# Performance work log

Measured on AMD Instinct MI355X. Metric: run time of the kernel, lower is better.

Reference implementation:

```python
import jax, jax.numpy as jnp
import numpy as np

B, L, D, H, DH = 2, 2048, 768, 12, 3072
HD = D // H          # head dim = 64
EPS = 1e-6
SCALE = float(np.sqrt(HD))


def setup_inputs() -> dict:
    key = jax.random.key(0)
    ks = jax.random.split(key, 24)
    w = lambda k, shape: jax.random.normal(k, shape, jnp.float32) * 0.02
    # RoPE angles: [L, HD//2]
    inv_freq = 1.0 / (10000.0 ** (jnp.arange(HD // 2, dtype=jnp.float32) / (HD // 2)))
    ang = jnp.arange(L, dtype=jnp.float32)[:, None] * inv_freq[None, :]
    return {
        "x": jax.random.normal(ks[0], (B, L, D), jnp.float32),
        "c": jax.random.normal(ks[1], (B, D), jnp.float32),
        "freqs_cos": jnp.cos(ang),
        "freqs_sin": jnp.sin(ang),
        "W_q": w(ks[2], (D, D)), "W_k": w(ks[3], (D, D)),
        "W_v": w(ks[4], (D, D)), "W_o": w(ks[5], (D, D)),
        "cond_w1": w(ks[6], (D, DH)), "cond_b1": jnp.zeros((DH,), jnp.float32),
        "cond_w2": w(ks[7], (DH, D)), "cond_b2": jnp.zeros((D,), jnp.float32),
        "attn_norm_w": jnp.ones((D,), jnp.float32),
        "attn_alpha": w(ks[8], (D, D)), "attn_beta": w(ks[9], (D, D)),
        "attn_gamma": w(ks[10], (D, D)),
        "ffn_gate": w(ks[11], (D, DH)), "ffn_hidden": w(ks[12], (D, DH)),
        "ffn_out": w(ks[13], (DH, D)),
        "ffn_norm_w": jnp.ones((D,), jnp.float32),
        "ffn_beta": w(ks[14], (D, D)), "ffn_gamma": w(ks[15], (D, D)),
    }


def _rms_norm(x, w):
    return w * x * jax.lax.rsqrt(jnp.mean(x * x, axis=-1, keepdims=True) + EPS)


def _rope(x, cos, sin):
    # x: [b, n, l, hd]; complex pairs are consecutive (even, odd) lanes
    x0, x1 = x[..., 0::2], x[..., 1::2]
    c, s = cos[None, None], sin[None, None]          # [1,1,l,hd//2]
    r0 = x0 * c - x1 * s
    r1 = x0 * s + x1 * c
    return jnp.stack([r0, r1], axis=-1).reshape(x.shape)


def _attention(h, cos, sin, W_q, W_k, W_v, W_o):
    b, l, d = h.shape
    split = lambda y: y.reshape(b, l, H, HD).transpose(0, 2, 1, 3)  # b n l hd
    q = _rope(split(h @ W_q), cos, sin)
    k = _rope(split(h @ W_k), cos, sin)
    v = split(h @ W_v)
    scores = jnp.einsum("bnld,bnmd->bnlm", q, k) / SCALE
    attn = jax.nn.softmax(scores, axis=-1)
    o = jnp.einsum("bnlm,bnmd->bnld", attn, v)
    return o.transpose(0, 2, 1, 3).reshape(b, l, d) @ W_o


def reference(x, c, freqs_cos, freqs_sin, W_q, W_k, W_v, W_o,
              cond_w1, cond_b1, cond_w2, cond_b2,
              attn_norm_w, attn_alpha, attn_beta, attn_gamma,
              ffn_gate, ffn_hidden, ffn_out, ffn_norm_w, ffn_beta, ffn_gamma):
    # conditioning embedding
    c2 = jax.nn.silu(c @ cond_w1 + cond_b1) @ cond_w2 + cond_b2   # [b, d]
    mod = lambda W: (c2 @ W)[:, None]                              # [b, 1, d]
    # attention sub-block with AdaLN modulation + alpha gating
    h = _rms_norm(x, attn_norm_w) * mod(attn_gamma) + mod(attn_beta)
    x = x + _attention(h, freqs_cos, freqs_sin, W_q, W_k, W_v, W_o) * mod(attn_alpha)
    # SwiGLU FFN sub-block (original gates the residual by ffn_gamma, not alpha)
    h = _rms_norm(x, ffn_norm_w) * mod(ffn_gamma) + mod(ffn_beta)
    ff = (jax.nn.silu(h @ ffn_gate) * (h @ ffn_hidden)) @ ffn_out
    return x + ff * mod(ffn_gamma)
```

## Files before the change

### kernel.cpp

```cpp
#include <hip/hip_runtime.h>

typedef unsigned short u16;
typedef __attribute__((ext_vector_type(8))) short short8;
typedef __attribute__((ext_vector_type(4))) float f32x4;

#define L_SEQ 2048
#define NHEAD 12
#define KVB 128
#define QBLK 128

__device__ __forceinline__ u16 f2bf(float f) {
    union { float f; unsigned u; } x; x.f = f;
    unsigned r = x.u + 0x7fffu + ((x.u >> 16) & 1u);
    return (u16)(r >> 16);
}
__device__ __forceinline__ float bf2f(u16 u) {
    union { unsigned u; float f; } x; x.u = ((unsigned)u) << 16;
    return x.f;
}
__device__ __forceinline__ float silu_f(float x) { return x / (1.f + __expf(-x)); }

__device__ __forceinline__ void gload16(const u16* g, u16* l) {
    __builtin_amdgcn_global_load_lds(
        (const __attribute__((address_space(1))) void*)g,
        (__attribute__((address_space(3))) void*)l, 16, 0, 0);
}

__global__ __launch_bounds__(256) void transpose_all(
    const float* __restrict__ S0, const float* __restrict__ S1,
    const float* __restrict__ S2, const float* __restrict__ S3,
    const float* __restrict__ S4, const float* __restrict__ S5,
    const float* __restrict__ S6,
    u16* __restrict__ D0, u16* __restrict__ D1, u16* __restrict__ D2,
    u16* __restrict__ D3, u16* __restrict__ D4, u16* __restrict__ D5,
    u16* __restrict__ D6)
{
    int id = blockIdx.x;
    const float* W; u16* Wt; int K, N, local;
    if (id < 2304) {
        int sec = id / 576; local = id - sec * 576; K = 768; N = 768;
        W  = (sec == 0) ? S0 : (sec == 1) ? S1 : (sec == 2) ? S2 : S3;
        Wt = (sec == 0) ? D0 : (sec == 1) ? D1 : (sec == 2) ? D2 : D3;
    } else if (id < 6912) {
        int sec = (id - 2304) / 2304; local = (id - 2304) - sec * 2304; K = 768; N = 3072;
        W = sec ? S5 : S4; Wt = sec ? D5 : D4;
    } else {
        local = id - 6912; K = 3072; N = 768; W = S6; Wt = D6;
    }
    int nx = N >> 5;
    int n0 = (local % nx) * 32, k0 = (local / nx) * 32;
    __shared__ float t[32][33];
    int tx = threadIdx.x & 31, ty = threadIdx.x >> 5;
#pragma unroll
    for (int i = 0; i < 4; i++)
        t[ty + 8 * i][tx] = W[(size_t)(k0 + ty + 8 * i) * N + n0 + tx];
    __syncthreads();
#pragma unroll
    for (int i = 0; i < 4; i++)
        Wt[(size_t)(n0 + ty + 8 * i) * K + k0 + tx] = f2bf(t[tx][ty + 8 * i]);
}

__global__ __launch_bounds__(256) void cond_mlp1(
    const float* __restrict__ c, const float* __restrict__ w1, float* __restrict__ part)
{
    int j = blockIdx.x * 256 + threadIdx.x;
    int d0 = blockIdx.y * 96;
    float a0 = 0.f, a1 = 0.f;
    for (int d = d0; d < d0 + 96; ++d) {
        float w = w1[(size_t)d * 3072 + j];
        a0 += c[d] * w;
        a1 += c[768 + d] * w;
    }
    part[(size_t)(blockIdx.y * 2 + 0) * 3072 + j] = a0;
    part[(size_t)(blockIdx.y * 2 + 1) * 3072 + j] = a1;
}

__global__ __launch_bounds__(256) void cond_mlp2(
    const float* __restrict__ part, const float* __restrict__ b1,
    const float* __restrict__ w2, float* __restrict__ c2part)
{
    __shared__ float hid[2][384];
    const int tid = threadIdx.x;
    const int d0 = blockIdx.y * 384;
    for (int i = tid; i < 768; i += 256) {
        int b = i / 384, dd = i - b * 384;
        float s = b1[d0 + dd];
#pragma unroll
        for (int p = 0; p < 8; p++) s += part[(size_t)(p * 2 + b) * 3072 + d0 + dd];
        hid[b][dd] = silu_f(s);
    }
    __syncthreads();
    int jj = tid & 63, kc = tid >> 6;
    int j = blockIdx.x * 64 + jj;
    float a0 = 0.f, a1 = 0.f;
    for (int dd = kc * 96; dd < kc * 96 + 96; ++dd) {
        float w = w2[(size_t)(d0 + dd) * 768 + j];
        a0 += hid[0][dd] * w;
        a1 += hid[1][dd] * w;
    }
    __shared__ float r0[256], r1[256];
    r0[tid] = a0; r1[tid] = a1;
    __syncthreads();
    if (kc == 0) {
        a0 = r0[jj] + r0[64 + jj] + r0[128 + jj] + r0[192 + jj];
        a1 = r1[jj] + r1[64 + jj] + r1[128 + jj] + r1[192 + jj];
        c2part[(size_t)(blockIdx.y * 2 + 0) * 768 + j] = a0;
        c2part[(size_t)(blockIdx.y * 2 + 1) * 768 + j] = a1;
    }
}

__global__ __launch_bounds__(256) void mod_gemm(
    const float* __restrict__ c2part, const float* __restrict__ b2,
    const float* __restrict__ W0, const float* __restrict__ W1,
    const float* __restrict__ W2, const float* __restrict__ W3,
    const float* __restrict__ W4, float* __restrict__ out)
{
    __shared__ float c2s[2][768];
    const int tid = threadIdx.x;
    for (int i = tid; i < 1536; i += 256) {
        int b = i / 768, d = i - b * 768;
        float s = b2[d];
#pragma unroll
        for (int p = 0; p < 8; p++) s += c2part[(size_t)(p * 2 + b) * 768 + d];
        c2s[b][d] = s;
    }
    __syncthreads();
    int w = blockIdx.y;
    const float* W = (w == 0) ? W0 : (w == 1) ? W1 : (w == 2) ? W2 : (w == 3) ? W3 : W4;
    int jj = tid & 63, kc = tid >> 6;
    int j = blockIdx.x * 64 + jj;
    float a0 = 0.f, a1 = 0.f;
    for (int d = kc * 192; d < kc * 192 + 192; ++d) {
        float ww = W[(size_t)d * 768 + j];
        a0 += c2s[0][d] * ww;
        a1 += c2s[1][d] * ww;
    }
    __shared__ float r0[256], r1[256];
    r0[tid] = a0; r1[tid] = a1;
    __syncthreads();
    if (kc == 0) {
        a0 = r0[jj] + r0[64 + jj] + r0[128 + jj] + r0[192 + jj];
        a1 = r1[jj] + r1[64 + jj] + r1[128 + jj] + r1[192 + jj];
        out[(size_t)(w * 2 + 0) * 768 + j] = a0;
        out[(size_t)(w * 2 + 1) * 768 + j] = a1;
    }
}

__global__ __launch_bounds__(256) void rmsnorm_mod(
    const float* __restrict__ xin, const float* __restrict__ nw,
    const float* __restrict__ gamma, const float* __restrict__ beta,
    u16* __restrict__ hout)
{
    int row = blockIdx.x;
    int b = row >> 11;
    const float* xr = xin + (size_t)row * 768;
    int t = threadIdx.x;
    float v0 = xr[t], v1 = xr[t + 256], v2 = xr[t + 512];
    float ss = v0 * v0 + v1 * v1 + v2 * v2;
#pragma unroll
    for (int m = 1; m < 64; m <<= 1) ss += __shfl_xor(ss, m);
    __shared__ float red[4];
    if ((t & 63) == 0) red[t >> 6] = ss;
    __syncthreads();
    float tot = red[0] + red[1] + red[2] + red[3];
    float rr = rsqrtf(tot * (1.f / 768.f) + 1e-6f);
    u16* ho = hout + (size_t)row * 768;
    const float* g = gamma + (size_t)b * 768;
    const float* be = beta + (size_t)b * 768;
#pragma unroll
    for (int i = 0; i < 3; i++) {
        int col = t + i * 256;
        float v = (i == 0) ? v0 : (i == 1) ? v1 : v2;
        ho[col] = f2bf(v * rr * nw[col] * g[col] + be[col]);
    }
}

template<int BM, int WM, int MODE, int LBX>
__global__ __launch_bounds__(256) void gemm_bf16(
    const u16* __restrict__ A, const u16* __restrict__ Bt,
    float* __restrict__ Cf, u16* __restrict__ Cb,
    const float* __restrict__ X, const float* __restrict__ coef,
    int M, int N, int K)
{
    constexpr int MR = WM / 16, NR = 4;
    __shared__ __align__(16) u16 As[2][BM * 32];
    __shared__ __align__(16) u16 Bs[2][128 * 32];
    const int lid = blockIdx.x;
    const int xcd = lid & 7, li = lid >> 3;
    const int bxi = xcd * (1 << LBX) + (li & ((1 << LBX) - 1));
    const int byi = li >> LBX;
    const int tid = threadIdx.x;
    const int lane = tid & 63, wid = tid >> 6;
    const int lo = lane & 15, hi = lane >> 4;
    const int bm = bxi * BM, bn = byi * 128;
    const int wrow = (wid >> 1) * WM, wcol = (wid & 1) * 64;

    f32x4 acc[MR][NR];
#pragma unroll
    for (int a = 0; a < MR; a++)
#pragma unroll
        for (int b = 0; b < NR; b++)
            acc[a][b] = (f32x4){0.f, 0.f, 0.f, 0.f};

    auto stage = [&](int buf, int k0) {
#pragma unroll
        for (int p = 0; p < BM / 64; p++) {
            int ch = tid + p * 256;
            gload16(A + (size_t)(bm + (ch >> 2)) * K + k0 + (ch & 3) * 8, &As[buf][ch * 8]);
        }
#pragma unroll
        for (int p = 0; p < 2; p++) {
            int ch = tid + p * 256;
            gload16(Bt + (size_t)(bn + (ch >> 2)) * K + k0 + (ch & 3) * 8, &Bs[buf][ch * 8]);
        }
    };

    stage(0, 0);
    int cur = 0;
    const int NT = K >> 5;
    for (int t = 0; t < NT; t++) {
        __syncthreads();
        if (t + 1 < NT) stage(cur ^ 1, (t + 1) * 32);
        short8 af[MR], bfr[NR];
#pragma unroll
        for (int mi = 0; mi < MR; mi++)
            af[mi] = *(const short8*)(&As[cur][(wrow + mi * 16 + lo) * 32 + hi * 8]);
#pragma unroll
        for (int nj = 0; nj < NR; nj++)
            bfr[nj] = *(const short8*)(&Bs[cur][(wcol + nj * 16 + lo) * 32 + hi * 8]);
        __builtin_amdgcn_s_setprio(1);
#pragma unroll
        for (int mi = 0; mi < MR; mi++)
#pragma unroll
            for (int nj = 0; nj < NR; nj++)
                acc[mi][nj] = __builtin_amdgcn_mfma_f32_16x16x32_bf16(af[mi], bfr[nj], acc[mi][nj], 0, 0, 0);
        __builtin_amdgcn_s_setprio(0);
        cur ^= 1;
    }
#pragma unroll
    for (int mi = 0; mi < MR; mi++)
#pragma unroll
        for (int nj = 0; nj < NR; nj++)
#pragma unroll
            for (int i = 0; i < 4; i++) {
                int row = bm + wrow + mi * 16 + hi * 4 + i;
                int col = bn + wcol + nj * 16 + lo;
                size_t idx = (size_t)row * N + col;
                float v = acc[mi][nj][i];
                if (MODE == 1) {
                    Cb[idx] = f2bf(v);
                } else {
                    int b = row >> 11;
                    Cf[idx] = X[idx] + v * coef[(size_t)b * N + col];
                }
            }
}

__global__ __launch_bounds__(256) void gemm_ffn1(
    const u16* __restrict__ A, const u16* __restrict__ Gt, const u16* __restrict__ Ht,
    u16* __restrict__ ff, int M, int N, int K)
{
    __shared__ __align__(16) u16 As[2][128 * 32];
    __shared__ __align__(16) u16 Gs[2][64 * 32];
    __shared__ __align__(16) u16 Hs[2][64 * 32];
    const int lid = blockIdx.x;
    const int xcd = lid & 7, li = lid >> 3;
    const int bxi = xcd * 4 + (li & 3);
    const int byi = li >> 2;
    const int tid = threadIdx.x;
    const int lane = tid & 63, wid = tid >> 6;
    const int lo = lane & 15, hi = lane >> 4;
    const int bm = bxi * 128, bn = byi * 64;
    const int wrow = (wid >> 1) * 64, wcol = (wid & 1) * 32;

    f32x4 ag[4][2], ah[4][2];
#pragma unroll
    for (int a = 0; a < 4; a++)
#pragma unroll
        for (int b = 0; b < 2; b++) {
            ag[a][b] = (f32x4){0.f, 0.f, 0.f, 0.f};
            ah[a][b] = (f32x4){0.f, 0.f, 0.f, 0.f};
        }

    auto stage = [&](int buf, int k0) {
#pragma unroll
        for (int p = 0; p < 2; p++) {
            int ch = tid + p * 256;
            gload16(A + (size_t)(bm + (ch >> 2)) * K + k0 + (ch & 3) * 8, &As[buf][ch * 8]);
        }
        {
            int ch = tid;
            gload16(Gt + (size_t)(bn + (ch >> 2)) * K + k0 + (ch & 3) * 8, &Gs[buf][ch * 8]);
            gload16(Ht + (size_t)(bn + (ch >> 2)) * K + k0 + (ch & 3) * 8, &Hs[buf][ch * 8]);
        }
    };

    stage(0, 0);
    int cur = 0;
    const int NT = K >> 5;
    for (int t = 0; t < NT; t++) {
        __syncthreads();
        if (t + 1 < NT) stage(cur ^ 1, (t + 1) * 32);
        short8 af[4], gf[2], hf[2];
#pragma unroll
        for (int mi = 0; mi < 4; mi++)
            af[mi] = *(const short8*)(&As[cur][(wrow + mi * 16 + lo) * 32 + hi * 8]);
#pragma unroll
        for (int nj = 0; nj < 2; nj++) {
            gf[nj] = *(const short8*)(&Gs[cur][(wcol + nj * 16 + lo) * 32 + hi * 8]);
            hf[nj] = *(const short8*)(&Hs[cur][(wcol + nj * 16 + lo) * 32 + hi * 8]);
        }
        __builtin_amdgcn_s_setprio(1);
#pragma unroll
        for (int mi = 0; mi < 4; mi++)
#pragma unroll
            for (int nj = 0; nj < 2; nj++) {
                ag[mi][nj] = __builtin_amdgcn_mfma_f32_16x16x32_bf16(af[mi], gf[nj], ag[mi][nj], 0, 0, 0);
                ah[mi][nj] = __builtin_amdgcn_mfma_f32_16x16x32_bf16(af[mi], hf[nj], ah[mi][nj], 0, 0, 0);
            }
        __builtin_amdgcn_s_setprio(0);
        cur ^= 1;
    }
#pragma unroll
    for (int mi = 0; mi < 4; mi++)
#pragma unroll
        for (int nj = 0; nj < 2; nj++)
#pragma unroll
            for (int i = 0; i < 4; i++) {
                int row = bm + wrow + mi * 16 + hi * 4 + i;
                int col = bn + wcol + nj * 16 + lo;
                ff[(size_t)row * N + col] = f2bf(silu_f(ag[mi][nj][i]) * ah[mi][nj][i]);
            }
}

__global__ __launch_bounds__(256) void rope_reshape(
    const u16* __restrict__ qr, const u16* __restrict__ kr, const u16* __restrict__ vr,
    const float* __restrict__ fc, const float* __restrict__ fs,
    u16* __restrict__ qo, u16* __restrict__ ko, u16* __restrict__ vt)
{
    const float QSCALE = 0.125f * 1.44269504f;
    __shared__ u16 Vl[64 * 64];
    const int tid = threadIdx.x;
    const int bh = blockIdx.y, lt = blockIdx.x;
    const int b = bh / NHEAD, h = bh % NHEAD;
    const int l0 = lt * 64;
    const int lrow = tid >> 2, ch = tid & 3;

    const size_t srow = ((size_t)(b * L_SEQ + l0 + lrow)) * 2304 + h * 64 + ch * 16;
    const size_t drow = ((size_t)(bh * L_SEQ + l0 + lrow)) * 64 + ch * 16;

    float cs[8], sn[8];
#pragma unroll
    for (int i = 0; i < 8; i++) {
        cs[i] = fc[(l0 + lrow) * 32 + ch * 8 + i];
        sn[i] = fs[(l0 + lrow) * 32 + ch * 8 + i];
    }
    union { int4 v4[2]; u16 s[16]; } iv, ov;
    iv.v4[0] = *(const int4*)(qr + srow); iv.v4[1] = *(const int4*)(qr + srow + 8);
#pragma unroll
    for (int i = 0; i < 8; i++) {
        float x0 = bf2f(iv.s[2 * i]), x1 = bf2f(iv.s[2 * i + 1]);
        ov.s[2 * i]     = f2bf((x0 * cs[i] - x1 * sn[i]) * QSCALE);
        ov.s[2 * i + 1] = f2bf((x0 * sn[i] + x1 * cs[i]) * QSCALE);
    }
    *(int4*)(qo + drow) = ov.v4[0]; *(int4*)(qo + drow + 8) = ov.v4[1];
    iv.v4[0] = *(const int4*)(kr + srow); iv.v4[1] = *(const int4*)(kr + srow + 8);
#pragma unroll
    for (int i = 0; i < 8; i++) {
        float x0 = bf2f(iv.s[2 * i]), x1 = bf2f(iv.s[2 * i + 1]);
        ov.s[2 * i]     = f2bf(x0 * cs[i] - x1 * sn[i]);
        ov.s[2 * i + 1] = f2bf(x0 * sn[i] + x1 * cs[i]);
    }
    *(int4*)(ko + drow) = ov.v4[0]; *(int4*)(ko + drow + 8) = ov.v4[1];
    iv.v4[0] = *(const int4*)(vr + srow); iv.v4[1] = *(const int4*)(vr + srow + 8);
#pragma unroll
    for (int e = 0; e < 16; e++) {
        int d = ch * 16 + e;
        Vl[d * 64 + (lrow ^ (((d >> 3) & 7) << 3))] = iv.s[e];
    }
    __syncthreads();
    const int d = tid >> 2;
    const int key = ((d >> 3) & 7) << 3;
    int4 o0 = *(const int4*)(&Vl[d * 64 + ((ch * 16) ^ key)]);
    int4 o1 = *(const int4*)(&Vl[d * 64 + ((ch * 16 + 8) ^ key)]);
    u16* vd = vt + ((size_t)bh * 64 + d) * L_SEQ + l0 + ch * 16;
    *(int4*)(vd) = o0; *(int4*)(vd + 8) = o1;
}

__global__ __launch_bounds__(512) void attn_fwd(
    const u16* __restrict__ q, const u16* __restrict__ k, const u16* __restrict__ vt,
    u16* __restrict__ outp)
{
    __shared__ __align__(16) u16 Kb[KVB * 64];
    __shared__ __align__(16) u16 Vb[64 * KVB];
    __shared__ __align__(16) u16 Ps[8][16 * KVB];
    const int tid = threadIdx.x;
    const int lane = tid & 63, wid = tid >> 6;
    const int lo = lane & 15, hi = lane >> 4;
    const int lid = blockIdx.x;
    const int xcd = lid & 7, li = lid >> 3;
    const int bh = xcd * 3 + (li >> 4);
    const int qt = li & 15;
    const int b = bh / NHEAD, h = bh % NHEAD;
    const int q0 = qt * QBLK + wid * 16;
    const u16* qb = q + ((size_t)bh * L_SEQ + q0) * 64;
    const u16* kbase = k + (size_t)bh * L_SEQ * 64;
    const u16* vbase = vt + (size_t)bh * 64 * L_SEQ;

    short8 qa0 = *(const short8*)(qb + lo * 64 + hi * 8);
    short8 qa1 = *(const short8*)(qb + lo * 64 + 32 + hi * 8);

    f32x4 oacc[4];
#pragma unroll
    for (int dt = 0; dt < 4; dt++) oacc[dt] = (f32x4){0.f, 0.f, 0.f, 0.f};
    float m_ = -1e30f, ls = 0.f;

    const int rk = tid >> 3, gk = tid & 7;
    const u16* ka = kbase + (size_t)rk * 64 + ((gk ^ (rk & 7)) * 8);
    const int rv = tid >> 4, gv = tid & 15;
    const u16* va = vbase + (size_t)rv * L_SEQ + ((gv ^ (rv & 15)) * 8);
    u16* kdst = &Kb[tid * 8];
    u16* vdst = &Vb[tid * 8];

    int4 kr0, kr1, vr0, vr1;
    kr0 = *(const int4*)(ka);
    kr1 = *(const int4*)(ka + 4096);
    vr0 = *(const int4*)(va);
    vr1 = *(const int4*)(va + 65536);

    const int NT = L_SEQ / KVB;
    u16* pw = &Ps[wid][0];
    const int pkey = lo << 3;
    for (int t = 0; t < NT; t++) {
        __syncthreads();
        *(int4*)(kdst)        = kr0;
        *(int4*)(kdst + 4096) = kr1;
        *(int4*)(vdst)        = vr0;
        *(int4*)(vdst + 4096) = vr1;
        __syncthreads();
        if (t + 1 < NT) {
            int kv0 = (t + 1) * KVB;
            const u16* kan = ka + (size_t)kv0 * 64;
            const u16* van = va + kv0;
            kr0 = *(const int4*)(kan);
            kr1 = *(const int4*)(kan + 4096);
            vr0 = *(const int4*)(van);
            vr1 = *(const int4*)(van + 65536);
        }
        f32x4 s[8];
#pragma unroll
        for (int nt = 0; nt < 8; nt++) {
            int kr_ = nt * 16 + lo;
            const u16* kp = &Kb[kr_ * 64];
            int key = (kr_ & 7) << 3;
            short8 kf0 = *(const short8*)(kp + ((hi * 8) ^ key));
            short8 kf1 = *(const short8*)(kp + ((32 + hi * 8) ^ key));
            __builtin_amdgcn_s_setprio(1);
            f32x4 z = (f32x4){0.f, 0.f, 0.f, 0.f};
            z = __builtin_amdgcn_mfma_f32_16x16x32_bf16(kf0, qa0, z, 0, 0, 0);
            s[nt] = __builtin_amdgcn_mfma_f32_16x16x32_bf16(kf1, qa1, s[nt] = z, 0, 0, 0);
            __builtin_amdgcn_s_setprio(0);
        }
        float t0 = fmaxf(fmaxf(s[0][0], s[0][1]), fmaxf(s[0][2], s[0][3]));
        float t1 = fmaxf(fmaxf(s[1][0], s[1][1]), fmaxf(s[1][2], s[1][3]));
        float t2 = fmaxf(fmaxf(s[2][0], s[2][1]), fmaxf(s[2][2], s[2][3]));
        float t3 = fmaxf(fmaxf(s[3][0], s[3][1]), fmaxf(s[3][2], s[3][3]));
        float t4 = fmaxf(fmaxf(s[4][0], s[4][1]), fmaxf(s[4][2], s[4][3]));
        float t5 = fmaxf(fmaxf(s[5][0], s[5][1]), fmaxf(s[5][2], s[5][3]));
        float t6 = fmaxf(fmaxf(s[6][0], s[6][1]), fmaxf(s[6][2], s[6][3]));
        float t7 = fmaxf(fmaxf(s[7][0], s[7][1]), fmaxf(s[7][2], s[7][3]));
        float pmax = fmaxf(fmaxf(fmaxf(t0, t1), fmaxf(t2, t3)),
                           fmaxf(fmaxf(t4, t5), fmaxf(t6, t7)));
        pmax = fmaxf(pmax, __shfl_xor(pmax, 16));
        pmax = fmaxf(pmax, __shfl_xor(pmax, 32));
        if (!__all(pmax - m_ <= 8.f)) {
            float mn = fmaxf(m_, pmax);
            float al = exp2f(m_ - mn);
            m_ = mn;
            ls *= al;
#pragma unroll
            for (int dt = 0; dt < 4; dt++) oacc[dt] *= al;
        }
        float rsA = 0.f, rsB = 0.f, rsC = 0.f, rsD = 0.f;
#pragma unroll
        for (int nt = 0; nt < 8; nt++) {
            float p0 = exp2f(s[nt][0] - m_);
            float p1 = exp2f(s[nt][1] - m_);
            float p2 = exp2f(s[nt][2] - m_);
            float p3 = exp2f(s[nt][3] - m_);
            s[nt][0] = p0; s[nt][1] = p1; s[nt][2] = p2; s[nt][3] = p3;
            rsA += p0; rsB += p1; rsC += p2; rsD += p3;
        }
        ls += (rsA + rsB) + (rsC + rsD);
#pragma unroll
        for (int nt = 0; nt < 8; nt++) {
            unsigned w0, w1;
            asm("v_cvt_pk_bf16_f32 %0, %1, %2" : "=v"(w0) : "v"(s[nt][0]), "v"(s[nt][1]));
            asm("v_cvt_pk_bf16_f32 %0, %1, %2" : "=v"(w1) : "v"(s[nt][2]), "v"(s[nt][3]));
            uint2 pk2; pk2.x = w0; pk2.y = w1;
            *(uint2*)(pw + lo * KVB + ((nt * 16 + hi * 4) ^ pkey)) = pk2;
        }
        short8 pa0 = *(const short8*)(pw + lo * KVB + ((0 * 32 + hi * 8) ^ pkey));
        short8 pa1 = *(const short8*)(pw + lo * KVB + ((1 * 32 + hi * 8) ^ pkey));
        short8 pa2 = *(const short8*)(pw + lo * KVB + ((2 * 32 + hi * 8) ^ pkey));
        short8 pa3 = *(const short8*)(pw + lo * KVB + ((3 * 32 + hi * 8) ^ pkey));
#pragma unroll
        for (int dt = 0; dt < 4; dt++) {
            int vr_ = dt * 16 + lo;
            const u16* vp = &Vb[vr_ * KVB];
            int vkey = (vr_ & 15) << 3;
            short8 vf0 = *(const short8*)(vp + ((0 * 32 + hi * 8) ^ vkey));
            short8 vf1 = *(const short8*)(vp + ((1 * 32 + hi * 8) ^ vkey));
            short8 vf2 = *(const short8*)(vp + ((2 * 32 + hi * 8) ^ vkey));
            short8 vf3 = *(const short8*)(vp + ((3 * 32 + hi * 8) ^ vkey));
            __builtin_amdgcn_s_setprio(1);
            oacc[dt] = __builtin_amdgcn_mfma_f32_16x16x32_bf16(vf0, pa0, oacc[dt], 0, 0, 0);
            oacc[dt] = __builtin_amdgcn_mfma_f32_16x16x32_bf16(vf1, pa1, oacc[dt], 0, 0, 0);
            oacc[dt] = __builtin_amdgcn_mfma_f32_16x16x32_bf16(vf2, pa2, oacc[dt], 0, 0, 0);
            oacc[dt] = __builtin_amdgcn_mfma_f32_16x16x32_bf16(vf3, pa3, oacc[dt], 0, 0, 0);
            __builtin_amdgcn_s_setprio(0);
        }
    }
    ls += __shfl_xor(ls, 16);
    ls += __shfl_xor(ls, 32);
    float inv = 1.f / ls;
    int qrow = q0 + lo;
    u16* orow = outp + ((size_t)(b * L_SEQ + qrow)) * 768 + h * 64;
#pragma unroll
    for (int dt = 0; dt < 4; dt++) {
        unsigned w0, w1;
        float o0 = oacc[dt][0] * inv, o1 = oacc[dt][1] * inv;
        float o2 = oacc[dt][2] * inv, o3 = oacc[dt][3] * inv;
        asm("v_cvt_pk_bf16_f32 %0, %1, %2" : "=v"(w0) : "v"(o0), "v"(o1));
        asm("v_cvt_pk_bf16_f32 %0, %1, %2" : "=v"(w1) : "v"(o2), "v"(o3));
        uint2 pk2; pk2.x = w0; pk2.y = w1;
        *(uint2*)(orow + dt * 16 + hi * 4) = pk2;
    }
}

extern "C" void kernel_launch(void* const* d_in, const int* in_sizes, int n_in,
                              void* d_out, int out_size, void* d_ws, size_t ws_size,
                              hipStream_t stream)
{
    const float* x      = (const float*)d_in[0];
    const float* c      = (const float*)d_in[1];
    const float* fcos   = (const float*)d_in[2];
    const float* fsin   = (const float*)d_in[3];
    const float* Wq     = (const float*)d_in[4];
    const float* Wk     = (const float*)d_in[5];
    const float* Wv     = (const float*)d_in[6];
    const float* Wo     = (const float*)d_in[7];
    const float* cw1    = (const float*)d_in[8];
    const float* cb1    = (const float*)d_in[9];
    const float* cw2    = (const float*)d_in[10];
    const float* cb2    = (const float*)d_in[11];
    const float* anw    = (const float*)d_in[12];
    const float* Walpha = (const float*)d_in[13];
    const float* Wbeta  = (const float*)d_in[14];
    const float* Wgamma = (const float*)d_in[15];
    const float* Wgate  = (const float*)d_in[16];
    const float* Whid   = (const float*)d_in[17];
    const float* Wout   = (const float*)d_in[18];
    const float* fnw    = (const float*)d_in[19];
    const float* Wbetaf = (const float*)d_in[20];
    const float* Wgammaf= (const float*)d_in[21];

    const int M = 4096;
    char* ws = (char*)d_ws;
    size_t off = 0;
    auto alloc = [&](size_t bytes) -> char* {
        char* p = ws + off;
        off += (bytes + 255) & ~(size_t)255;
        return p;
    };
    u16* wq_t   = (u16*)alloc((size_t)768 * 768 * 2);
    u16* wk_t   = (u16*)alloc((size_t)768 * 768 * 2);
    u16* wv_t   = (u16*)alloc((size_t)768 * 768 * 2);
    u16* wo_t   = (u16*)alloc((size_t)768 * 768 * 2);
    u16* gate_t = (u16*)alloc((size_t)3072 * 768 * 2);
    u16* hid_t  = (u16*)alloc((size_t)3072 * 768 * 2);
    u16* out_t  = (u16*)alloc((size_t)768 * 3072 * 2);
    float* part1 = (float*)alloc((size_t)8 * 2 * 3072 * 4);
    float* part2 = (float*)alloc((size_t)8 * 2 * 768 * 4);
    float* mods = (float*)alloc(5 * 2 * 768 * 4);
    u16* hbuf   = (u16*)alloc((size_t)M * 768 * 2);
    u16* qkvraw = (u16*)alloc((size_t)M * 2304 * 2);
    u16* qrope  = (u16*)alloc((size_t)M * 768 * 2);
    u16* krope  = (u16*)alloc((size_t)M * 768 * 2);
    u16* vtb    = (u16*)alloc((size_t)M * 768 * 2);
    u16* attnh  = (u16*)alloc((size_t)M * 768 * 2);
    float* ybuf = (float*)alloc((size_t)M * 768 * 4);
    u16* ffbuf  = (u16*)alloc((size_t)M * 3072 * 2);

    transpose_all<<<9216, 256, 0, stream>>>(
        Wq, Wk, Wv, Wo, Wgate, Whid, Wout,
        wq_t, wk_t, wv_t, wo_t, gate_t, hid_t, out_t);

    cond_mlp1<<<dim3(12, 8), 256, 0, stream>>>(c, cw1, part1);
    cond_mlp2<<<dim3(12, 8), 256, 0, stream>>>(part1, cb1, cw2, part2);
    mod_gemm<<<dim3(12, 5), 256, 0, stream>>>(
        part2, cb2, Wgamma, Wbeta, Walpha, Wgammaf, Wbetaf, mods);

    rmsnorm_mod<<<M, 256, 0, stream>>>(x, anw, mods + 0 * 1536, mods + 1 * 1536, hbuf);

    gemm_bf16<128, 64, 1, 2><<<dim3(576), 256, 0, stream>>>(
        hbuf, wq_t, nullptr, qkvraw, nullptr, nullptr, M, 2304, 768);

    rope_reshape<<<dim3(32, 24), 256, 0, stream>>>(
        qkvraw, qkvraw + 768, qkvraw + 1536,
        fcos, fsin, qrope, krope, vtb);

    attn_fwd<<<dim3(384), 512, 0, stream>>>(qrope, krope, vtb, attnh);

    gemm_bf16<64, 32, 2, 3><<<dim3(384), 256, 0, stream>>>(
        attnh, wo_t, ybuf, nullptr, x, mods + 2 * 1536, M, 768, 768);

    rmsnorm_mod<<<M, 256, 0, stream>>>(ybuf, fnw, mods + 3 * 1536, mods + 4 * 1536, hbuf);

    gemm_ffn1<<<dim3(1536), 256, 0, stream>>>(
        hbuf, gate_t, hid_t, ffbuf, M, 3072, 768);

    gemm_bf16<64, 32, 2, 3><<<dim3(384), 256, 0, stream>>>(
        ffbuf, out_t, (float*)d_out, nullptr, ybuf, mods + 3 * 1536, M, 768, 3072);
}
```

Before: 261.0 us.

## Triple-buffer LDS staging in GEMM kernels with explicit vmcnt waits

Both the generic bf16 GEMM and the fused FFN gate/hidden GEMM move from double to triple-buffered LDS tiles. Loads are now issued two K-steps ahead. The full __syncthreads is replaced by raw s_barrier plus hand-counted s_waitcnt vmcnt values, so only the oldest stage's async global-to-LDS loads must finish before compute. This is meant to hide more global-memory latency behind MFMA work. The cost is 50% more shared memory per block, which may lower occupancy, and hardcoded wait counts that depend on the per-stage load count.

```diff
diff --git a/kernel.cpp b/kernel.cpp
--- a/kernel.cpp
+++ b/kernel.cpp
@@ -183,8 +183,9 @@
     int M, int N, int K)
 {
     constexpr int MR = WM / 16, NR = 4;
-    __shared__ __align__(16) u16 As[2][BM * 32];
-    __shared__ __align__(16) u16 Bs[2][128 * 32];
+    constexpr int LPT = BM / 64 + 2;
+    __shared__ __align__(16) u16 As[3][BM * 32];
+    __shared__ __align__(16) u16 Bs[3][128 * 32];
     const int lid = blockIdx.x;
     const int xcd = lid & 7, li = lid >> 3;
     const int bxi = xcd * (1 << LBX) + (li & ((1 << LBX) - 1));
@@ -215,12 +216,24 @@
         }
     };
 
+    const int NT = K >> 5;
     stage(0, 0);
+    stage(1, 32);
     int cur = 0;
-    const int NT = K >> 5;
     for (int t = 0; t < NT; t++) {
-        __syncthreads();
-        if (t + 1 < NT) stage(cur ^ 1, (t + 1) * 32);
+        __builtin_amdgcn_s_barrier();
+        int nxt = cur + 2; if (nxt >= 3) nxt -= 3;
+        if (t + 2 < NT) stage(nxt, (t + 2) * 32);
+        if (t + 2 < NT) {
+            if constexpr (LPT == 4) asm volatile("s_waitcnt vmcnt(8)" ::: "memory");
+            else                    asm volatile("s_waitcnt vmcnt(6)" ::: "memory");
+        } else if (t + 1 < NT) {
+            if constexpr (LPT == 4) asm volatile("s_waitcnt vmcnt(4)" ::: "memory");
+            else                    asm volatile("s_waitcnt vmcnt(3)" ::: "memory");
+        } else {
+            asm volatile("s_waitcnt vmcnt(0)" ::: "memory");
+        }
+        __builtin_amdgcn_s_barrier();
         short8 af[MR], bfr[NR];
 #pragma unroll
         for (int mi = 0; mi < MR; mi++)
@@ -235,7 +248,7 @@
             for (int nj = 0; nj < NR; nj++)
                 acc[mi][nj] = __builtin_amdgcn_mfma_f32_16x16x32_bf16(af[mi], bfr[nj], acc[mi][nj], 0, 0, 0);
         __builtin_amdgcn_s_setprio(0);
-        cur ^= 1;
+        cur = (cur == 2) ? 0 : cur + 1;
     }
 #pragma unroll
     for (int mi = 0; mi < MR; mi++)
@@ -260,9 +273,9 @@
     const u16* __restrict__ A, const u16* __restrict__ Gt, const u16* __restrict__ Ht,
     u16* __restrict__ ff, int M, int N, int K)
 {
-    __shared__ __align__(16) u16 As[2][128 * 32];
-    __shared__ __align__(16) u16 Gs[2][64 * 32];
-    __shared__ __align__(16) u16 Hs[2][64 * 32];
+    __shared__ __align__(16) u16 As[3][128 * 32];
+    __shared__ __align__(16) u16 Gs[3][64 * 32];
+    __shared__ __align__(16) u16 Hs[3][64 * 32];
     const int lid = blockIdx.x;
     const int xcd = lid & 7, li = lid >> 3;
     const int bxi = xcd * 4 + (li & 3);
@@ -295,12 +308,18 @@
         }
     };
 
+    const int NT = K >> 5;
     stage(0, 0);
+    stage(1, 32);
     int cur = 0;
-    const int NT = K >> 5;
     for (int t = 0; t < NT; t++) {
-        __syncthreads();
-        if (t + 1 < NT) stage(cur ^ 1, (t + 1) * 32);
+        __builtin_amdgcn_s_barrier();
+        int nxt = cur + 2; if (nxt >= 3) nxt -= 3;
+        if (t + 2 < NT) stage(nxt, (t + 2) * 32);
+        if (t + 2 < NT)      asm volatile("s_waitcnt vmcnt(8)" ::: "memory");
+        else if (t + 1 < NT) asm volatile("s_waitcnt vmcnt(4)" ::: "memory");
+        else                 asm volatile("s_waitcnt vmcnt(0)" ::: "memory");
+        __builtin_amdgcn_s_barrier();
         short8 af[4], gf[2], hf[2];
 #pragma unroll
         for (int mi = 0; mi < 4; mi++)
@@ -319,7 +338,7 @@
                 ah[mi][nj] = __builtin_amdgcn_mfma_f32_16x16x32_bf16(af[mi], hf[nj], ah[mi][nj], 0, 0, 0);
             }
         __builtin_amdgcn_s_setprio(0);
-        cur ^= 1;
+        cur = (cur == 2) ? 0 : cur + 1;
     }
 #pragma unroll
     for (int mi = 0; mi < 4; mi++)
```

Measured after the change: 261.2 us. No clear change (+0.1%).
